# Kernel tuning notes

Hardware: AMD Instinct MI355X
Metric: run time of the kernel (lower is better)

Reference implementation:

```python
import jax, jax.numpy as jnp
import numpy as np


def sinusoidal_pe(S, D, dtype):
    # standard transformer sinusoidal positional encoding, shape [S, D]
    pos = jnp.arange(S, dtype=jnp.float32)[:, None]
    div = jnp.exp(jnp.arange(0, D, 2, dtype=jnp.float32) * (-np.log(10000.0) / D))
    ang = pos * div  # [S, D/2]
    pe = jnp.zeros((S, D), jnp.float32)
    pe = pe.at[:, 0::2].set(jnp.sin(ang)).at[:, 1::2].set(jnp.cos(ang))
    return pe.astype(dtype)


def setup_inputs() -> dict:
    key = jax.random.key(0)
    k1, k2, k3, k4, k5 = jax.random.split(key, 5)
    B, S, F, D, SEG = 64, 512, 64, 1024, 8
    x = jax.random.normal(k1, (B, S, F), jnp.float32)
    W_emb = jax.random.normal(k2, (F, D), jnp.float32) / np.sqrt(F)
    b_emb = jax.random.normal(k3, (D,), jnp.float32) * 0.01
    w_seg = jax.random.normal(k4, (SEG,), jnp.float32) / np.sqrt(SEG)
    b_seg = jax.random.normal(k5, (1,), jnp.float32) * 0.01
    return {"x": x, "W_emb": W_emb, "b_emb": b_emb, "w_seg": w_seg, "b_seg": b_seg}


def reference(x, W_emb, b_emb, w_seg, b_seg):
    B, S, F = x.shape
    D = W_emb.shape[1]
    seg_len = w_seg.shape[0]  # seq_len divisible by seg_len -> pad_len == 0 branch
    # input token embedding
    x1 = x @ W_emb + b_emb  # [B, S, D]
    # segment embedding: tensor_split at multiples of seg_len == reshape,
    # Linear(seg_len, 1) over the time axis of each chunk, broadcast over chunk.
    xr = x1.reshape(B, S // seg_len, seg_len, D)
    seg = jnp.einsum('bnsd,s->bnd', xr, w_seg) + b_seg[0]  # [B, n_seg, D]
    x2 = (xr + seg[:, :, None, :]).reshape(B, S, D)
    # positional encoding added to x2
    return x2 + sinusoidal_pe(S, D, x2.dtype)
```

## Files before the change

### kernel.cpp

```cpp
#include <hip/hip_runtime.h>
#include <stdint.h>


typedef __attribute__((ext_vector_type(8))) short short8;
typedef __attribute__((ext_vector_type(4))) float f32x4;

#define D_DIM 1024
#define WS_PE_OFF 131072
#define WS_X_OFF (131072 + 2097152)

__device__ __forceinline__ unsigned short f2bf(float f) {
  unsigned u = __float_as_uint(f);
  u = (u + 0x7FFFu + ((u >> 16) & 1u)) >> 16;
  return (unsigned short)u;
}

__global__ __launch_bounds__(256) void bert_setup_kernel(
    const float* __restrict__ x, const float* __restrict__ W,
    const float* __restrict__ b_emb, const float* __restrict__ w_seg,
    const float* __restrict__ b_seg, unsigned short* __restrict__ wsW,
    float* __restrict__ wsPE, unsigned short* __restrict__ wsX) {
  const int bid = blockIdx.x;
  const int tid = threadIdx.x;
  if (bid < 1024) {
    const int t = bid * 256 + tid;
    const float4* p = reinterpret_cast<const float4*>(x) + (size_t)t * 2;
    float4 v0 = p[0], v1 = p[1];
    short8 o;
    o[0] = (short)f2bf(v0.x); o[1] = (short)f2bf(v0.y);
    o[2] = (short)f2bf(v0.z); o[3] = (short)f2bf(v0.w);
    o[4] = (short)f2bf(v1.x); o[5] = (short)f2bf(v1.y);
    o[6] = (short)f2bf(v1.z); o[7] = (short)f2bf(v1.w);
    *reinterpret_cast<short8*>(wsX + (size_t)t * 8) = o;
  } else if (bid < 3072) {
    const int t = (bid - 1024) * 256 + tid;
    const int s = t >> 10;
    const int c = t & 1023;
    float Sw = 0.f;
#pragma unroll
    for (int i = 0; i < 8; ++i) Sw += w_seg[i];
    const float inv2pi = 0.15915494309189535f;
    const float KLOG = 0.02595256324130752f;
    float divrev = exp2f(-(float)(c >> 1) * KLOG) * inv2pi;
    float rev = (float)s * divrev + ((c & 1) ? 0.25f : 0.f);
    rev = rev - floorf(rev);
    float pe = __builtin_amdgcn_sinf(rev);
    wsPE[t] = pe + b_emb[c] * (1.f + Sw) + b_seg[0];
  } else {
    const int t = (bid - 3072) * 256 + tid;
    const int cf = t >> 7;
    const int kf = (t >> 6) & 1;
    const int lane = t & 63;
    const int col = cf * 16 + (lane & 15);
    const int k0 = kf * 32 + ((lane >> 4) << 3);
    short8 o;
#pragma unroll
    for (int i = 0; i < 8; ++i)
      o[i] = (short)f2bf(W[(size_t)(k0 + i) * D_DIM + col]);
    *reinterpret_cast<short8*>(wsW + (size_t)t * 8) = o;
  }
}

__global__ __launch_bounds__(256) void bert_main_kernel(
    const unsigned short* __restrict__ wsX,
    const unsigned short* __restrict__ wsW, const float* __restrict__ wsPE,
    const float* __restrict__ w_seg, float* __restrict__ out) {
  const int tid = threadIdx.x;
  const int lane = tid & 63;
  const int wave = tid >> 6;
  const int bid = blockIdx.x;
  const int nblk = (bid >> 3) & 7;
  const int mblk = (bid & 7) | ((bid >> 6) << 3);
  const int mbase = mblk * 64;
  const int nbase = nblk * 128;
  const int mw = wave >> 1;
  const int nw = wave & 1;
  const int L15 = lane & 15;
  const int g = lane >> 4;

  short8 aW[4][2];
#pragma unroll
  for (int cf = 0; cf < 4; ++cf) {
#pragma unroll
    for (int kf = 0; kf < 2; ++kf) {
      const int cfg = (nbase >> 4) + nw * 4 + cf;
      aW[cf][kf] = *reinterpret_cast<const short8*>(
          wsW + ((size_t)(cfg * 2 + kf) * 64 + lane) * 8);
    }
  }

  short8 bX[2][2];
#pragma unroll
  for (int rf = 0; rf < 2; ++rf) {
#pragma unroll
    for (int kf = 0; kf < 2; ++kf) {
      const int row = mbase + mw * 32 + rf * 16 + L15;
      bX[rf][kf] = *reinterpret_cast<const short8*>(
          wsX + (size_t)row * 64 + kf * 32 + g * 8);
    }
  }

  f32x4 acc[4][2];
#pragma unroll
  for (int cf = 0; cf < 4; ++cf) {
#pragma unroll
    for (int rf = 0; rf < 2; ++rf) {
      f32x4 c = {0.f, 0.f, 0.f, 0.f};
      c = __builtin_amdgcn_mfma_f32_16x16x32_bf16(aW[cf][0], bX[rf][0], c, 0,
                                                  0, 0);
      c = __builtin_amdgcn_mfma_f32_16x16x32_bf16(aW[cf][1], bX[rf][1], c, 0,
                                                  0, 0);
      acc[cf][rf] = c;
    }
  }

  const float t = w_seg[lane & 7];

#pragma unroll
  for (int cf = 0; cf < 4; ++cf) {
#pragma unroll
    for (int rf = 0; rf < 2; ++rf) {
      f32x4 a = acc[cf][rf];
      float q0 = a[0] * t, q1 = a[1] * t, q2 = a[2] * t, q3 = a[3] * t;
      q0 += __shfl_xor(q0, 1); q1 += __shfl_xor(q1, 1);
      q2 += __shfl_xor(q2, 1); q3 += __shfl_xor(q3, 1);
      q0 += __shfl_xor(q0, 2); q1 += __shfl_xor(q1, 2);
      q2 += __shfl_xor(q2, 2); q3 += __shfl_xor(q3, 2);
      q0 += __shfl_xor(q0, 4); q1 += __shfl_xor(q1, 4);
      q2 += __shfl_xor(q2, 4); q3 += __shfl_xor(q3, 4);

      const int row = mbase + mw * 32 + rf * 16 + L15;
      const int s = row & 511;
      const int colq = nbase + nw * 64 + cf * 16 + g * 4;
      const float4 pe4 =
          *reinterpret_cast<const float4*>(wsPE + (size_t)s * D_DIM + colq);
      float4 o;
      o.x = a[0] + q0 + pe4.x;
      o.y = a[1] + q1 + pe4.y;
      o.z = a[2] + q2 + pe4.z;
      o.w = a[3] + q3 + pe4.w;
      *reinterpret_cast<float4*>(out + (size_t)row * D_DIM + colq) = o;
    }
  }
}

extern "C" void kernel_launch(void* const* d_in, const int* in_sizes, int n_in,
                              void* d_out, int out_size, void* d_ws,
                              size_t ws_size, hipStream_t stream) {
  const float* x = (const float*)d_in[0];
  const float* W = (const float*)d_in[1];
  const float* b_emb = (const float*)d_in[2];
  const float* w_seg = (const float*)d_in[3];
  const float* b_seg = (const float*)d_in[4];
  float* out = (float*)d_out;

  unsigned short* wsW = (unsigned short*)d_ws;
  float* wsPE = (float*)((char*)d_ws + WS_PE_OFF);
  unsigned short* wsX = (unsigned short*)((char*)d_ws + WS_X_OFF);

  bert_setup_kernel<<<3104, 256, 0, stream>>>(x, W, b_emb, w_seg, b_seg, wsW,
                                              wsPE, wsX);
  bert_main_kernel<<<4096, 256, 0, stream>>>(wsX, wsW, wsPE, w_seg, out);
}
```

Measured before the change: 46.86 us.

## Fuse x conversion and PE computation into persistent main kernel with LDS-staged stores

The setup kernel is reduced to W conversion only. The main kernel now converts x to bf16 in LDS, computes the sinusoidal PE and bias terms inline, and loops over four 32-row tiles per block with W fragments held in registers. Results are staged through swizzled LDS so each row is written with fully coalesced stores. This drops the workspace round trips for x and PE and cuts the grid to 512 blocks. The cost is more registers, extra sin work per element, and fewer blocks to hide latency.

```diff
diff --git a/kernel.cpp b/kernel.cpp
--- a/kernel.cpp
+++ b/kernel.cpp
@@ -6,8 +6,6 @@
 typedef __attribute__((ext_vector_type(4))) float f32x4;
 
 #define D_DIM 1024
-#define WS_PE_OFF 131072
-#define WS_X_OFF (131072 + 2097152)
 
 __device__ __forceinline__ unsigned short f2bf(float f) {
   unsigned u = __float_as_uint(f);
@@ -15,131 +13,147 @@
   return (unsigned short)u;
 }
 
-__global__ __launch_bounds__(256) void bert_setup_kernel(
-    const float* __restrict__ x, const float* __restrict__ W,
-    const float* __restrict__ b_emb, const float* __restrict__ w_seg,
-    const float* __restrict__ b_seg, unsigned short* __restrict__ wsW,
-    float* __restrict__ wsPE, unsigned short* __restrict__ wsX) {
-  const int bid = blockIdx.x;
-  const int tid = threadIdx.x;
-  if (bid < 1024) {
-    const int t = bid * 256 + tid;
-    const float4* p = reinterpret_cast<const float4*>(x) + (size_t)t * 2;
-    float4 v0 = p[0], v1 = p[1];
-    short8 o;
-    o[0] = (short)f2bf(v0.x); o[1] = (short)f2bf(v0.y);
-    o[2] = (short)f2bf(v0.z); o[3] = (short)f2bf(v0.w);
-    o[4] = (short)f2bf(v1.x); o[5] = (short)f2bf(v1.y);
-    o[6] = (short)f2bf(v1.z); o[7] = (short)f2bf(v1.w);
-    *reinterpret_cast<short8*>(wsX + (size_t)t * 8) = o;
-  } else if (bid < 3072) {
-    const int t = (bid - 1024) * 256 + tid;
-    const int s = t >> 10;
-    const int c = t & 1023;
-    float Sw = 0.f;
+__global__ __launch_bounds__(256) void bert_wconv(const float* __restrict__ W,
+                                                  unsigned short* __restrict__ wsW) {
+  const int t = blockIdx.x * 256 + threadIdx.x;
+  const int lane = t & 63;
+  const int kf = (t >> 6) & 1;
+  const int cfg = t >> 7;
+  const int col = cfg * 16 + (lane & 15);
+  const int k0 = kf * 32 + ((lane >> 4) << 3);
+  short8 o;
 #pragma unroll
-    for (int i = 0; i < 8; ++i) Sw += w_seg[i];
-    const float inv2pi = 0.15915494309189535f;
-    const float KLOG = 0.02595256324130752f;
-    float divrev = exp2f(-(float)(c >> 1) * KLOG) * inv2pi;
-    float rev = (float)s * divrev + ((c & 1) ? 0.25f : 0.f);
-    rev = rev - floorf(rev);
-    float pe = __builtin_amdgcn_sinf(rev);
-    wsPE[t] = pe + b_emb[c] * (1.f + Sw) + b_seg[0];
-  } else {
-    const int t = (bid - 3072) * 256 + tid;
-    const int cf = t >> 7;
-    const int kf = (t >> 6) & 1;
-    const int lane = t & 63;
-    const int col = cf * 16 + (lane & 15);
-    const int k0 = kf * 32 + ((lane >> 4) << 3);
-    short8 o;
-#pragma unroll
-    for (int i = 0; i < 8; ++i)
-      o[i] = (short)f2bf(W[(size_t)(k0 + i) * D_DIM + col]);
-    *reinterpret_cast<short8*>(wsW + (size_t)t * 8) = o;
-  }
+  for (int i = 0; i < 8; ++i)
+    o[i] = (short)f2bf(W[(size_t)(k0 + i) * D_DIM + col]);
+  *reinterpret_cast<short8*>(wsW + (size_t)t * 8) = o;
 }
 
-__global__ __launch_bounds__(256) void bert_main_kernel(
-    const unsigned short* __restrict__ wsX,
-    const unsigned short* __restrict__ wsW, const float* __restrict__ wsPE,
-    const float* __restrict__ w_seg, float* __restrict__ out) {
+__global__ __launch_bounds__(256, 2) void bert_main(
+    const float* __restrict__ x, const unsigned short* __restrict__ wsW,
+    const float* __restrict__ b_emb, const float* __restrict__ w_seg,
+    const float* __restrict__ b_seg, float* __restrict__ out) {
+  __shared__ unsigned short ldsx[32 * 64];
+  __shared__ float ldse[32 * 512];
+  char* const ldsxB = (char*)ldsx;
+  char* const ldseB = (char*)ldse;
+
   const int tid = threadIdx.x;
   const int lane = tid & 63;
-  const int wave = tid >> 6;
-  const int bid = blockIdx.x;
-  const int nblk = (bid >> 3) & 7;
-  const int mblk = (bid & 7) | ((bid >> 6) << 3);
-  const int mbase = mblk * 64;
-  const int nbase = nblk * 128;
-  const int mw = wave >> 1;
-  const int nw = wave & 1;
+  const int w = tid >> 6;
   const int L15 = lane & 15;
   const int g = lane >> 4;
+  const int h = blockIdx.x & 1;
+  const int rg = blockIdx.x >> 1;
+  const int wcol = h * 512 + w * 128;
 
-  short8 aW[4][2];
+  short8 aW[8][2];
 #pragma unroll
-  for (int cf = 0; cf < 4; ++cf) {
+  for (int cf = 0; cf < 8; ++cf)
 #pragma unroll
-    for (int kf = 0; kf < 2; ++kf) {
-      const int cfg = (nbase >> 4) + nw * 4 + cf;
+    for (int kf = 0; kf < 2; ++kf)
       aW[cf][kf] = *reinterpret_cast<const short8*>(
-          wsW + ((size_t)(cfg * 2 + kf) * 64 + lane) * 8);
-    }
+          wsW + ((size_t)(((wcol >> 4) + cf) * 2 + kf) * 64 + lane) * 8);
+
+  float Sw = 0.f;
+#pragma unroll
+  for (int i = 0; i < 8; ++i) Sw += w_seg[i];
+  const float s1w = 1.f + Sw;
+  const float bseg = b_seg[0];
+  const float tseg = w_seg[L15 & 7];
+
+  const float inv2pi = 0.15915494309189535f;
+  const float KLOG = 0.02595256324130752f;
+  float divr[8][2];
+#pragma unroll
+  for (int cf = 0; cf < 8; ++cf) {
+    const int p = (wcol + cf * 16 + g * 4) >> 1;
+    divr[cf][0] = exp2f(-(float)p * KLOG) * inv2pi;
+    divr[cf][1] = exp2f(-(float)(p + 1) * KLOG) * inv2pi;
   }
 
-  short8 bX[2][2];
+  for (int it = 0; it < 4; ++it) {
+    const int rbase = rg * 128 + it * 32;
+
+    {
+      const int r = tid >> 3;
+      const int c8 = (tid & 7) * 8;
+      const float* xp = x + (size_t)(rbase + r) * 64 + c8;
+      const float4 v0 = *reinterpret_cast<const float4*>(xp);
+      const float4 v1 = *reinterpret_cast<const float4*>(xp + 4);
+      short8 o;
+      o[0] = (short)f2bf(v0.x); o[1] = (short)f2bf(v0.y);
+      o[2] = (short)f2bf(v0.z); o[3] = (short)f2bf(v0.w);
+      o[4] = (short)f2bf(v1.x); o[5] = (short)f2bf(v1.y);
+      o[6] = (short)f2bf(v1.z); o[7] = (short)f2bf(v1.w);
+      *reinterpret_cast<short8*>(
+          ldsxB + ((r * 128 + c8 * 2) ^ ((r & 7) << 4))) = o;
+    }
+    __syncthreads();
+
+    short8 bX[2][2];
 #pragma unroll
-  for (int rf = 0; rf < 2; ++rf) {
+    for (int rf = 0; rf < 2; ++rf)
 #pragma unroll
-    for (int kf = 0; kf < 2; ++kf) {
-      const int row = mbase + mw * 32 + rf * 16 + L15;
-      bX[rf][kf] = *reinterpret_cast<const short8*>(
-          wsX + (size_t)row * 64 + kf * 32 + g * 8);
-    }
-  }
+      for (int kf = 0; kf < 2; ++kf) {
+        const int r = rf * 16 + L15;
+        bX[rf][kf] = *reinterpret_cast<const short8*>(
+            ldsxB + ((r * 128 + kf * 64 + g * 16) ^ ((r & 7) << 4)));
+      }
 
-  f32x4 acc[4][2];
+    f32x4 acc[8][2];
 #pragma unroll
-  for (int cf = 0; cf < 4; ++cf) {
+    for (int cf = 0; cf < 8; ++cf)
 #pragma unroll
-    for (int rf = 0; rf < 2; ++rf) {
-      f32x4 c = {0.f, 0.f, 0.f, 0.f};
-      c = __builtin_amdgcn_mfma_f32_16x16x32_bf16(aW[cf][0], bX[rf][0], c, 0,
-                                                  0, 0);
-      c = __builtin_amdgcn_mfma_f32_16x16x32_bf16(aW[cf][1], bX[rf][1], c, 0,
-                                                  0, 0);
-      acc[cf][rf] = c;
-    }
-  }
-
-  const float t = w_seg[lane & 7];
+      for (int rf = 0; rf < 2; ++rf) {
+        f32x4 c = {0.f, 0.f, 0.f, 0.f};
+        c = __builtin_amdgcn_mfma_f32_16x16x32_bf16(aW[cf][0], bX[rf][0], c, 0, 0, 0);
+        c = __builtin_amdgcn_mfma_f32_16x16x32_bf16(aW[cf][1], bX[rf][1], c, 0, 0, 0);
+        acc[cf][rf] = c;
+      }
 
 #pragma unroll
-  for (int cf = 0; cf < 4; ++cf) {
+    for (int cf = 0; cf < 8; ++cf) {
+      const int c0 = wcol + cf * 16 + g * 4;
+      const float4 eb = *reinterpret_cast<const float4*>(b_emb + c0);
 #pragma unroll
-    for (int rf = 0; rf < 2; ++rf) {
-      f32x4 a = acc[cf][rf];
-      float q0 = a[0] * t, q1 = a[1] * t, q2 = a[2] * t, q3 = a[3] * t;
-      q0 += __shfl_xor(q0, 1); q1 += __shfl_xor(q1, 1);
-      q2 += __shfl_xor(q2, 1); q3 += __shfl_xor(q3, 1);
-      q0 += __shfl_xor(q0, 2); q1 += __shfl_xor(q1, 2);
-      q2 += __shfl_xor(q2, 2); q3 += __shfl_xor(q3, 2);
-      q0 += __shfl_xor(q0, 4); q1 += __shfl_xor(q1, 4);
-      q2 += __shfl_xor(q2, 4); q3 += __shfl_xor(q3, 4);
+      for (int rf = 0; rf < 2; ++rf) {
+        f32x4 a = acc[cf][rf];
+        float q0 = a[0] * tseg, q1 = a[1] * tseg, q2 = a[2] * tseg, q3 = a[3] * tseg;
+        q0 += __shfl_xor(q0, 1); q1 += __shfl_xor(q1, 1);
+        q2 += __shfl_xor(q2, 1); q3 += __shfl_xor(q3, 1);
+        q0 += __shfl_xor(q0, 2); q1 += __shfl_xor(q1, 2);
+        q2 += __shfl_xor(q2, 2); q3 += __shfl_xor(q3, 2);
+        q0 += __shfl_xor(q0, 4); q1 += __shfl_xor(q1, 4);
+        q2 += __shfl_xor(q2, 4); q3 += __shfl_xor(q3, 4);
 
-      const int row = mbase + mw * 32 + rf * 16 + L15;
-      const int s = row & 511;
-      const int colq = nbase + nw * 64 + cf * 16 + g * 4;
-      const float4 pe4 =
-          *reinterpret_cast<const float4*>(wsPE + (size_t)s * D_DIM + colq);
-      float4 o;
-      o.x = a[0] + q0 + pe4.x;
-      o.y = a[1] + q1 + pe4.y;
-      o.z = a[2] + q2 + pe4.z;
-      o.w = a[3] + q3 + pe4.w;
-      *reinterpret_cast<float4*>(out + (size_t)row * D_DIM + colq) = o;
+        const int r = rf * 16 + L15;
+        const float s = (float)((rbase + r) & 511);
+        const float pe0 = __builtin_amdgcn_sinf(__builtin_amdgcn_fractf(s * divr[cf][0]));
+        const float pe1 = __builtin_amdgcn_sinf(__builtin_amdgcn_fractf(s * divr[cf][0] + 0.25f));
+        const float pe2 = __builtin_amdgcn_sinf(__builtin_amdgcn_fractf(s * divr[cf][1]));
+        const float pe3 = __builtin_amdgcn_sinf(__builtin_amdgcn_fractf(s * divr[cf][1] + 0.25f));
+
+        f32x4 o;
+        o[0] = a[0] + q0 + pe0 + eb.x * s1w + bseg;
+        o[1] = a[1] + q1 + pe1 + eb.y * s1w + bseg;
+        o[2] = a[2] + q2 + pe2 + eb.z * s1w + bseg;
+        o[3] = a[3] + q3 + pe3 + eb.w * s1w + bseg;
+
+        const int colh = w * 128 + cf * 16 + g * 4;
+        *reinterpret_cast<f32x4*>(
+            ldseB + (((r * 512 + colh) * 4) ^ ((r & 7) << 4))) = o;
+      }
+    }
+    __syncthreads();
+
+#pragma unroll
+    for (int p = 0; p < 16; ++p) {
+      const int flat = p * 1024 + tid * 4;
+      const int r = flat >> 9;
+      const int c = flat & 511;
+      const f32x4 v = *reinterpret_cast<const f32x4*>(
+          ldseB + ((flat * 4) ^ ((r & 7) << 4)));
+      *reinterpret_cast<f32x4*>(out + (size_t)(rbase + r) * D_DIM + h * 512 + c) = v;
     }
   }
 }
@@ -153,12 +167,8 @@
   const float* w_seg = (const float*)d_in[3];
   const float* b_seg = (const float*)d_in[4];
   float* out = (float*)d_out;
+  unsigned short* wsW = (unsigned short*)d_ws;
 
-  unsigned short* wsW = (unsigned short*)d_ws;
-  float* wsPE = (float*)((char*)d_ws + WS_PE_OFF);
-  unsigned short* wsX = (unsigned short*)((char*)d_ws + WS_X_OFF);
-
-  bert_setup_kernel<<<3104, 256, 0, stream>>>(x, W, b_emb, w_seg, b_seg, wsW,
-                                              wsPE, wsX);
-  bert_main_kernel<<<4096, 256, 0, stream>>>(wsX, wsW, wsPE, w_seg, out);
+  bert_wconv<<<32, 256, 0, stream>>>(W, wsW);
+  bert_main<<<512, 256, 0, stream>>>(x, wsW, b_emb, w_seg, b_seg, out);
 }
```

Result: slower. 59.70 us (+27.4%).
